# Performance work log

Measured on AMD Instinct MI355X. Metric: run time of the kernel, lower is better.

## Reference

```python
import jax, jax.numpy as jnp
import numpy as np

N_NODES = 100000   # type_num + rel_num
TYPE_NUM = 80000
EMB_DIM = 64
DIM1 = 64
DIM2 = 64
N_EDGES = 1_600_000


def _gcn_conv(x, W, b, src, dst, norm, n):
    # PyG GCNConv: h = x @ W, then symmetric-normalized aggregation, then bias
    h = x @ W                              # [n, out]
    msgs = norm[:, None] * h[src]          # [e, out] gather
    out = jax.ops.segment_sum(msgs, dst, num_segments=n)  # scatter-add
    return out + b


def setup_inputs() -> dict:
    key = jax.random.key(0)
    k0, k1, k2, k3 = jax.random.split(key, 4)
    # xavier-uniform style scales
    def xavier(k, shape):
        fan_in, fan_out = shape[-2], shape[-1]
        lim = float(np.sqrt(6.0 / (fan_in + fan_out)))
        return jax.random.uniform(k, shape, jnp.float32, -lim, lim)
    node_emb = xavier(k0, (N_NODES, EMB_DIM))
    W1 = xavier(k1, (EMB_DIM, DIM1))
    b1 = jnp.zeros((DIM1,), jnp.float32)
    W2 = xavier(k2, (DIM1, DIM2))
    b2 = jnp.zeros((DIM2,), jnp.float32)
    edge_index = jax.random.randint(k3, (2, N_EDGES), 0, N_NODES, dtype=jnp.int32)
    return {"node_emb": node_emb, "W1": W1, "b1": b1, "W2": W2, "b2": b2,
            "edge_index": edge_index}


def reference(node_emb, W1, b1, W2, b2, edge_index):
    n = node_emb.shape[0]
    # GCNConv default: add self-loops, symmetric normalization D^-1/2 (A+I) D^-1/2
    loops = jnp.arange(n, dtype=edge_index.dtype)
    src = jnp.concatenate([edge_index[0], loops])
    dst = jnp.concatenate([edge_index[1], loops])
    deg = jax.ops.segment_sum(jnp.ones_like(dst, dtype=node_emb.dtype), dst,
                              num_segments=n)
    dinv = jnp.where(deg > 0, jax.lax.rsqrt(deg), 0.0)
    norm = dinv[src] * dinv[dst]           # [e+n]
    X = jax.nn.relu(_gcn_conv(node_emb, W1, b1, src, dst, norm, n))
    X = jax.nn.relu(_gcn_conv(X, W2, b2, src, dst, norm, n))
    return X[:TYPE_NUM], X[TYPE_NUM:]
```

## Files before the change

kernel.cpp:

```cpp
#include <hip/hip_runtime.h>
#include <hip/hip_bf16.h>


#define BSH   7
#define BMSK  127
#define CAPE  2592
#define EPB   8192

__global__ __launch_bounds__(256) void k_part(const int* __restrict__ src,
                                              const int* __restrict__ dst,
                                              int* __restrict__ bcur,
                                              unsigned* __restrict__ tpack,
                                              int ne, int nb) {
    __shared__ int lh[800], lbase[800], lrk[800];
    for (int t = threadIdx.x; t < nb; t += 256) { lh[t] = 0; lrk[t] = 0; }
    __syncthreads();
    const int beg = blockIdx.x * EPB;
    const int end = min(beg + EPB, ne);
    for (int e = beg + threadIdx.x * 4; e < end; e += 1024) {
        if (e + 3 < end) {
            int4 d = *(const int4*)(dst + e);
            atomicAdd(&lh[d.x >> BSH], 1);
            atomicAdd(&lh[d.y >> BSH], 1);
            atomicAdd(&lh[d.z >> BSH], 1);
            atomicAdd(&lh[d.w >> BSH], 1);
        } else {
            for (int q = e; q < end; ++q) atomicAdd(&lh[dst[q] >> BSH], 1);
        }
    }
    __syncthreads();
    for (int t = threadIdx.x; t < nb; t += 256)
        lbase[t] = lh[t] ? atomicAdd(&bcur[t], lh[t]) : 0;
    __syncthreads();
    for (int e = beg + threadIdx.x * 4; e < end; e += 1024) {
        if (e + 3 < end) {
            int4 d4 = *(const int4*)(dst + e);
            int4 s4 = *(const int4*)(src + e);
            int b, r, pos;
            b = d4.x >> BSH; r = atomicAdd(&lrk[b], 1); pos = lbase[b] + r;
            if (pos < CAPE) tpack[(size_t)b * CAPE + pos] = (unsigned)s4.x | ((unsigned)(d4.x & BMSK) << 17);
            b = d4.y >> BSH; r = atomicAdd(&lrk[b], 1); pos = lbase[b] + r;
            if (pos < CAPE) tpack[(size_t)b * CAPE + pos] = (unsigned)s4.y | ((unsigned)(d4.y & BMSK) << 17);
            b = d4.z >> BSH; r = atomicAdd(&lrk[b], 1); pos = lbase[b] + r;
            if (pos < CAPE) tpack[(size_t)b * CAPE + pos] = (unsigned)s4.z | ((unsigned)(d4.z & BMSK) << 17);
            b = d4.w >> BSH; r = atomicAdd(&lrk[b], 1); pos = lbase[b] + r;
            if (pos < CAPE) tpack[(size_t)b * CAPE + pos] = (unsigned)s4.w | ((unsigned)(d4.w & BMSK) << 17);
        } else {
            for (int q = e; q < end; ++q) {
                int d = dst[q], s = src[q];
                int b = d >> BSH;
                int r = atomicAdd(&lrk[b], 1);
                int pos = lbase[b] + r;
                if (pos < CAPE) tpack[(size_t)b * CAPE + pos] = (unsigned)s | ((unsigned)(d & BMSK) << 17);
            }
        }
    }
}

__global__ __launch_bounds__(256) void k_bin(const unsigned* __restrict__ tpack,
                                             const int* __restrict__ bcur,
                                             int* __restrict__ offsets,
                                             int* __restrict__ ecnt,
                                             float* __restrict__ dinv,
                                             unsigned* __restrict__ ssort,
                                             const float* __restrict__ emb,
                                             float* __restrict__ Xe, int n) {
    __shared__ int hist[128], loff[128], cur[128];
    __shared__ float ldv[128];
    const int b = blockIdx.x;
    const int cnt = min(bcur[b], CAPE);
    const int dbase = b << BSH;
    const unsigned* tp = tpack + (size_t)b * CAPE;
    if (threadIdx.x < 128) { hist[threadIdx.x] = 0; cur[threadIdx.x] = 0; }
    __syncthreads();
    for (int e = threadIdx.x; e < cnt; e += 256)
        atomicAdd(&hist[tp[e] >> 17], 1);
    __syncthreads();
    if (threadIdx.x < 64) {
        const int lane = threadIdx.x;
        int v0 = hist[lane], v1 = hist[64 + lane];
        int x0 = v0, x1 = v1;
        #pragma unroll
        for (int off = 1; off < 64; off <<= 1) {
            int t0 = __shfl_up(x0, off); if (lane >= off) x0 += t0;
            int t1 = __shfl_up(x1, off); if (lane >= off) x1 += t1;
        }
        int sum0 = __shfl(x0, 63);
        loff[lane]      = x0 - v0;
        loff[64 + lane] = sum0 + x1 - v1;
    }
    __syncthreads();
    if (threadIdx.x < 128) {
        const int d = dbase + threadIdx.x;
        const float dv = rsqrtf((float)(hist[threadIdx.x] + 1));
        ldv[threadIdx.x] = dv;
        if (d < n) {
            offsets[d] = b * CAPE + loff[threadIdx.x];
            ecnt[d]    = hist[threadIdx.x];
            dinv[d]    = dv;
        }
    }
    __syncthreads();
    {
        const float4* ev = (const float4*)(emb + (size_t)dbase * 64);
        float4*       xv = (float4*)(Xe + (size_t)dbase * 64);
        const int lim = min(n - dbase, 128) * 16;
        for (int idx = threadIdx.x; idx < lim; idx += 256) {
            const float dv = ldv[idx >> 4];
            float4 v = ev[idx];
            v.x *= dv; v.y *= dv; v.z *= dv; v.w *= dv;
            xv[idx] = v;
        }
    }
    unsigned* sb = ssort + (size_t)b * CAPE;
    for (int e = threadIdx.x; e < cnt; e += 256) {
        unsigned p = tp[e];
        int dl = (int)(p >> 17);
        int r  = atomicAdd(&cur[dl], 1);
        sb[loff[dl] + r] = p & 0x1FFFFu;
    }
}

__global__ __launch_bounds__(256) void k_agg(const float* __restrict__ X,
                                             const int* __restrict__ offsets,
                                             const int* __restrict__ ecnt,
                                             const unsigned* __restrict__ ssort,
                                             const float* __restrict__ dinv,
                                             float* __restrict__ Y, int n) {
    __shared__ unsigned sw[16][48];
    const int g  = threadIdx.x >> 4;
    const int fl = threadIdx.x & 15;
    const int f0 = fl * 4;
    const int i  = blockIdx.x * 16 + g;
    if (i >= n) return;
    const int beg = offsets[i];
    const int cnt = ecnt[i];
    const float di = dinv[i];
    float4 acc = {0.f, 0.f, 0.f, 0.f};
    for (int cb = 0; cb < cnt; cb += 32) {
        const int ccnt = min(cnt - cb, 32);
        {
            const int t0 = fl, t1 = fl + 16;
            sw[g][t0] = (t0 < ccnt) ? ssort[beg + cb + t0] : 0u;
            sw[g][t1] = (t1 < ccnt) ? ssort[beg + cb + t1] : 0u;
        }
        for (int jb = 0; jb < ccnt; jb += 8) {
            unsigned p[8];
            #pragma unroll
            for (int u = 0; u < 8; ++u) p[u] = sw[g][jb + u];
            float4 h[8];
            #pragma unroll
            for (int u = 0; u < 8; ++u)
                h[u] = *(const float4*)(X + (size_t)p[u] * 64 + f0);
            #pragma unroll
            for (int u = 0; u < 8; ++u) {
                const float w = (jb + u < ccnt) ? 1.f : 0.f;
                acc.x = fmaf(w, h[u].x, acc.x);
                acc.y = fmaf(w, h[u].y, acc.y);
                acc.z = fmaf(w, h[u].z, acc.z);
                acc.w = fmaf(w, h[u].w, acc.w);
            }
        }
    }
    const float4 xs = *(const float4*)(X + (size_t)i * 64 + f0);
    acc.x = di * (acc.x + xs.x);
    acc.y = di * (acc.y + xs.y);
    acc.z = di * (acc.z + xs.z);
    acc.w = di * (acc.w + xs.w);
    *(float4*)(Y + (size_t)i * 64 + f0) = acc;
}

#define GEMM_ACC(ai, xi)                                                  \
    ai.x = fmaf(xi.x, w0.x, ai.x); ai.y = fmaf(xi.x, w0.y, ai.y);         \
    ai.z = fmaf(xi.x, w0.z, ai.z); ai.w = fmaf(xi.x, w0.w, ai.w);         \
    ai.x = fmaf(xi.y, w1.x, ai.x); ai.y = fmaf(xi.y, w1.y, ai.y);         \
    ai.z = fmaf(xi.y, w1.z, ai.z); ai.w = fmaf(xi.y, w1.w, ai.w);         \
    ai.x = fmaf(xi.z, w2.x, ai.x); ai.y = fmaf(xi.z, w2.y, ai.y);         \
    ai.z = fmaf(xi.z, w2.z, ai.z); ai.w = fmaf(xi.z, w2.w, ai.w);         \
    ai.x = fmaf(xi.w, w3.x, ai.x); ai.y = fmaf(xi.w, w3.y, ai.y);         \
    ai.z = fmaf(xi.w, w3.z, ai.z); ai.w = fmaf(xi.w, w3.w, ai.w);

#define GEMM_STORE(ai, idx)                                               \
    if (r0 + idx < n) {                                                   \
        float4 r;                                                         \
        r.x = fmaxf(ai.x + bv.x, 0.f); r.y = fmaxf(ai.y + bv.y, 0.f);     \
        r.z = fmaxf(ai.z + bv.z, 0.f); r.w = fmaxf(ai.w + bv.w, 0.f);     \
        if (SCALE) {                                                      \
            const float sc = rscale[r0 + idx];                            \
            r.x *= sc; r.y *= sc; r.z *= sc; r.w *= sc;                   \
        }                                                                 \
        *(float4*)(H + (size_t)(r0 + idx) * 64 + c0) = r;                 \
    }

template<bool SCALE>
__global__ __launch_bounds__(256, 4) void k_gemm64(const float* __restrict__ X,
                                                   const float* __restrict__ W,
                                                   const float* __restrict__ bias,
                                                   const float* __restrict__ rscale,
                                                   float* __restrict__ H, int n) {
    __shared__ float Wl[64 * 64];
    {
        const float4* Wv = (const float4*)W;
        float4* Wlv = (float4*)Wl;
        for (int t = threadIdx.x; t < 1024; t += 256) Wlv[t] = Wv[t];
    }
    __syncthreads();
    const int cg = threadIdx.x & 15;
    const int rg = threadIdx.x >> 4;
    const int c0 = cg * 4;
    const float4 bv = *(const float4*)(bias + c0);
    const int ntile = (n + 63) >> 6;
    for (int t = blockIdx.x; t < ntile; t += gridDim.x) {
        const int r0 = t * 64 + rg * 4;
        const float* xp0 = X + (size_t)min(r0 + 0, n - 1) * 64;
        const float* xp1 = X + (size_t)min(r0 + 1, n - 1) * 64;
        const float* xp2 = X + (size_t)min(r0 + 2, n - 1) * 64;
        const float* xp3 = X + (size_t)min(r0 + 3, n - 1) * 64;
        float4 a0 = {0,0,0,0}, a1 = {0,0,0,0}, a2 = {0,0,0,0}, a3 = {0,0,0,0};
        #pragma unroll 4
        for (int k = 0; k < 64; k += 4) {
            const float4 x0 = *(const float4*)(xp0 + k);
            const float4 x1 = *(const float4*)(xp1 + k);
            const float4 x2 = *(const float4*)(xp2 + k);
            const float4 x3 = *(const float4*)(xp3 + k);
            const float4 w0 = *(const float4*)(&Wl[(k + 0) * 64 + c0]);
            const float4 w1 = *(const float4*)(&Wl[(k + 1) * 64 + c0]);
            const float4 w2 = *(const float4*)(&Wl[(k + 2) * 64 + c0]);
            const float4 w3 = *(const float4*)(&Wl[(k + 3) * 64 + c0]);
            GEMM_ACC(a0, x0)
            GEMM_ACC(a1, x1)
            GEMM_ACC(a2, x2)
            GEMM_ACC(a3, x3)
        }
        GEMM_STORE(a0, 0)
        GEMM_STORE(a1, 1)
        GEMM_STORE(a2, 2)
        GEMM_STORE(a3, 3)
    }
}

extern "C" void kernel_launch(void* const* d_in, const int* in_sizes, int n_in,
                              void* d_out, int out_size, void* d_ws, size_t ws_size,
                              hipStream_t stream) {
    const float* emb = (const float*)d_in[0];
    const float* W1  = (const float*)d_in[1];
    const float* b1  = (const float*)d_in[2];
    const float* W2  = (const float*)d_in[3];
    const float* b2  = (const float*)d_in[4];
    const int*   ei  = (const int*)d_in[5];

    const int n  = in_sizes[0] / 64;
    const int ne = in_sizes[5] / 2;
    const int* src = ei;
    const int* dst = ei + ne;
    const int nb = (n + BMSK) >> BSH;

    char* ws = (char*)d_ws;
    size_t off = 0;
    auto alloc = [&](size_t bytes) { void* p = ws + off; off = (off + bytes + 63) & ~size_t(63); return p; };
    int*      bcur    = (int*)     alloc((size_t)nb * 4);
    int*      offsets = (int*)     alloc((size_t)n * 4);
    int*      ecnt    = (int*)     alloc((size_t)n * 4);
    float*    dinv    = (float*)   alloc((size_t)n * 4);
    unsigned* ssort   = (unsigned*)alloc((size_t)nb * CAPE * 4);
    size_t ybytes = (size_t)n * 64 * 4;
    size_t tbytes = (size_t)nb * CAPE * 4;
    void* yt = alloc(ybytes > tbytes ? ybytes : tbytes);
    unsigned* tpack = (unsigned*)yt;
    float*    Y     = (float*)yt;
    (void)ws_size;

    float* out = (float*)d_out;

    hipMemsetAsync(bcur, 0, (size_t)nb * 4, stream);

    const int pb = (ne + EPB - 1) / EPB;
    const int wb = (n + 15) / 16;
    const int gb = min((n + 63) / 64, 2048);

    k_part<<<pb, 256, 0, stream>>>(src, dst, bcur, tpack, ne, nb);
    k_bin <<<nb, 256, 0, stream>>>(tpack, bcur, offsets, ecnt, dinv, ssort,
                                   emb, out, n);

    k_agg<<<wb, 256, 0, stream>>>(out, offsets, ecnt, ssort, dinv, Y, n);
    k_gemm64<true><<<gb, 256, 0, stream>>>(Y, W1, b1, dinv, out, n);
    k_agg<<<wb, 256, 0, stream>>>(out, offsets, ecnt, ssort, dinv, Y, n);
    k_gemm64<false><<<gb, 256, 0, stream>>>(Y, W2, b2, nullptr, out, n);
}
```

Baseline: 208.3 us.

## Fuse neighbor aggregation with dense 64x64 transform in one kernel per layer

Merges the gather-aggregation kernel and the GEMM kernel into a single 1024-thread kernel per layer. The aggregated rows stay in shared memory and are multiplied by the weight tile loaded there, so the intermediate Y buffer is never written to or read back from global memory, and two launches are removed. In exchange, blocks are larger and carry more shared memory (weights, row tile and index staging), which can lower occupancy. The wave-skewed edge loop now sits before a block-wide barrier, so uneven degrees within a block leave threads idle.

```diff
diff --git a/kernel.cpp b/kernel.cpp
--- a/kernel.cpp
+++ b/kernel.cpp
@@ -121,121 +121,93 @@
     }
 }
 
-__global__ __launch_bounds__(256) void k_agg(const float* __restrict__ X,
-                                             const int* __restrict__ offsets,
-                                             const int* __restrict__ ecnt,
-                                             const unsigned* __restrict__ ssort,
-                                             const float* __restrict__ dinv,
-                                             float* __restrict__ Y, int n) {
-    __shared__ unsigned sw[16][48];
+template<bool SCALE>
+__global__ __launch_bounds__(1024, 8)
+void k_fused(const float* __restrict__ X,
+             const float* __restrict__ W,
+             const float* __restrict__ bias,
+             const float* __restrict__ rscale,
+             const int* __restrict__ offsets,
+             const int* __restrict__ ecnt,
+             const unsigned* __restrict__ ssort,
+             const float* __restrict__ dinv,
+             float* __restrict__ H, int n) {
+    __shared__ float    Wl[64 * 64];
+    __shared__ float    Xs[64][68];
+    __shared__ unsigned sw[64][48];
+    {
+        const float4* Wv = (const float4*)W;
+        float4* Wlv = (float4*)Wl;
+        Wlv[threadIdx.x] = Wv[threadIdx.x];
+    }
     const int g  = threadIdx.x >> 4;
     const int fl = threadIdx.x & 15;
     const int f0 = fl * 4;
-    const int i  = blockIdx.x * 16 + g;
-    if (i >= n) return;
-    const int beg = offsets[i];
-    const int cnt = ecnt[i];
-    const float di = dinv[i];
+    const int i  = blockIdx.x * 64 + g;
+
     float4 acc = {0.f, 0.f, 0.f, 0.f};
-    for (int cb = 0; cb < cnt; cb += 32) {
-        const int ccnt = min(cnt - cb, 32);
-        {
-            const int t0 = fl, t1 = fl + 16;
-            sw[g][t0] = (t0 < ccnt) ? ssort[beg + cb + t0] : 0u;
-            sw[g][t1] = (t1 < ccnt) ? ssort[beg + cb + t1] : 0u;
-        }
-        for (int jb = 0; jb < ccnt; jb += 8) {
-            unsigned p[8];
-            #pragma unroll
-            for (int u = 0; u < 8; ++u) p[u] = sw[g][jb + u];
-            float4 h[8];
-            #pragma unroll
-            for (int u = 0; u < 8; ++u)
-                h[u] = *(const float4*)(X + (size_t)p[u] * 64 + f0);
-            #pragma unroll
-            for (int u = 0; u < 8; ++u) {
-                const float w = (jb + u < ccnt) ? 1.f : 0.f;
-                acc.x = fmaf(w, h[u].x, acc.x);
-                acc.y = fmaf(w, h[u].y, acc.y);
-                acc.z = fmaf(w, h[u].z, acc.z);
-                acc.w = fmaf(w, h[u].w, acc.w);
+    if (i < n) {
+        const int beg = offsets[i];
+        const int cnt = ecnt[i];
+        const float di = dinv[i];
+        for (int cb = 0; cb < cnt; cb += 32) {
+            const int ccnt = min(cnt - cb, 32);
+            sw[g][fl]      = (fl      < ccnt) ? ssort[beg + cb + fl]      : 0u;
+            sw[g][fl + 16] = (fl + 16 < ccnt) ? ssort[beg + cb + fl + 16] : 0u;
+            for (int jb = 0; jb < ccnt; jb += 8) {
+                unsigned p[8];
+                #pragma unroll
+                for (int u = 0; u < 8; ++u) p[u] = sw[g][jb + u];
+                float4 h[8];
+                #pragma unroll
+                for (int u = 0; u < 8; ++u)
+                    h[u] = *(const float4*)(X + (size_t)p[u] * 64 + f0);
+                #pragma unroll
+                for (int u = 0; u < 8; ++u) {
+                    const float w = (jb + u < ccnt) ? 1.f : 0.f;
+                    acc.x = fmaf(w, h[u].x, acc.x);
+                    acc.y = fmaf(w, h[u].y, acc.y);
+                    acc.z = fmaf(w, h[u].z, acc.z);
+                    acc.w = fmaf(w, h[u].w, acc.w);
+                }
             }
         }
-    }
-    const float4 xs = *(const float4*)(X + (size_t)i * 64 + f0);
-    acc.x = di * (acc.x + xs.x);
-    acc.y = di * (acc.y + xs.y);
-    acc.z = di * (acc.z + xs.z);
-    acc.w = di * (acc.w + xs.w);
-    *(float4*)(Y + (size_t)i * 64 + f0) = acc;
-}
-
-#define GEMM_ACC(ai, xi)                                                  \
-    ai.x = fmaf(xi.x, w0.x, ai.x); ai.y = fmaf(xi.x, w0.y, ai.y);         \
-    ai.z = fmaf(xi.x, w0.z, ai.z); ai.w = fmaf(xi.x, w0.w, ai.w);         \
-    ai.x = fmaf(xi.y, w1.x, ai.x); ai.y = fmaf(xi.y, w1.y, ai.y);         \
-    ai.z = fmaf(xi.y, w1.z, ai.z); ai.w = fmaf(xi.y, w1.w, ai.w);         \
-    ai.x = fmaf(xi.z, w2.x, ai.x); ai.y = fmaf(xi.z, w2.y, ai.y);         \
-    ai.z = fmaf(xi.z, w2.z, ai.z); ai.w = fmaf(xi.z, w2.w, ai.w);         \
-    ai.x = fmaf(xi.w, w3.x, ai.x); ai.y = fmaf(xi.w, w3.y, ai.y);         \
-    ai.z = fmaf(xi.w, w3.z, ai.z); ai.w = fmaf(xi.w, w3.w, ai.w);
-
-#define GEMM_STORE(ai, idx)                                               \
-    if (r0 + idx < n) {                                                   \
-        float4 r;                                                         \
-        r.x = fmaxf(ai.x + bv.x, 0.f); r.y = fmaxf(ai.y + bv.y, 0.f);     \
-        r.z = fmaxf(ai.z + bv.z, 0.f); r.w = fmaxf(ai.w + bv.w, 0.f);     \
-        if (SCALE) {                                                      \
-            const float sc = rscale[r0 + idx];                            \
-            r.x *= sc; r.y *= sc; r.z *= sc; r.w *= sc;                   \
-        }                                                                 \
-        *(float4*)(H + (size_t)(r0 + idx) * 64 + c0) = r;                 \
-    }
-
-template<bool SCALE>
-__global__ __launch_bounds__(256, 4) void k_gemm64(const float* __restrict__ X,
-                                                   const float* __restrict__ W,
-                                                   const float* __restrict__ bias,
-                                                   const float* __restrict__ rscale,
-                                                   float* __restrict__ H, int n) {
-    __shared__ float Wl[64 * 64];
-    {
-        const float4* Wv = (const float4*)W;
-        float4* Wlv = (float4*)Wl;
-        for (int t = threadIdx.x; t < 1024; t += 256) Wlv[t] = Wv[t];
-    }
-    __syncthreads();
-    const int cg = threadIdx.x & 15;
-    const int rg = threadIdx.x >> 4;
-    const int c0 = cg * 4;
-    const float4 bv = *(const float4*)(bias + c0);
-    const int ntile = (n + 63) >> 6;
-    for (int t = blockIdx.x; t < ntile; t += gridDim.x) {
-        const int r0 = t * 64 + rg * 4;
-        const float* xp0 = X + (size_t)min(r0 + 0, n - 1) * 64;
-        const float* xp1 = X + (size_t)min(r0 + 1, n - 1) * 64;
-        const float* xp2 = X + (size_t)min(r0 + 2, n - 1) * 64;
-        const float* xp3 = X + (size_t)min(r0 + 3, n - 1) * 64;
-        float4 a0 = {0,0,0,0}, a1 = {0,0,0,0}, a2 = {0,0,0,0}, a3 = {0,0,0,0};
-        #pragma unroll 4
-        for (int k = 0; k < 64; k += 4) {
-            const float4 x0 = *(const float4*)(xp0 + k);
-            const float4 x1 = *(const float4*)(xp1 + k);
-            const float4 x2 = *(const float4*)(xp2 + k);
-            const float4 x3 = *(const float4*)(xp3 + k);
-            const float4 w0 = *(const float4*)(&Wl[(k + 0) * 64 + c0]);
-            const float4 w1 = *(const float4*)(&Wl[(k + 1) * 64 + c0]);
-            const float4 w2 = *(const float4*)(&Wl[(k + 2) * 64 + c0]);
-            const float4 w3 = *(const float4*)(&Wl[(k + 3) * 64 + c0]);
-            GEMM_ACC(a0, x0)
-            GEMM_ACC(a1, x1)
-            GEMM_ACC(a2, x2)
-            GEMM_ACC(a3, x3)
-        }
-        GEMM_STORE(a0, 0)
-        GEMM_STORE(a1, 1)
-        GEMM_STORE(a2, 2)
-        GEMM_STORE(a3, 3)
+        const float4 xs = *(const float4*)(X + (size_t)i * 64 + f0);
+        acc.x = di * (acc.x + xs.x);
+        acc.y = di * (acc.y + xs.y);
+        acc.z = di * (acc.z + xs.z);
+        acc.w = di * (acc.w + xs.w);
+    }
+    *(float4*)(&Xs[g][f0]) = acc;
+    __syncthreads();
+
+    const float4 bv = *(const float4*)(bias + f0);
+    float4 a = {0.f, 0.f, 0.f, 0.f};
+    #pragma unroll 4
+    for (int k = 0; k < 64; k += 4) {
+        const float4 x4 = *(const float4*)(&Xs[g][k]);
+        const float4 w0 = *(const float4*)(&Wl[(k + 0) * 64 + f0]);
+        const float4 w1 = *(const float4*)(&Wl[(k + 1) * 64 + f0]);
+        const float4 w2 = *(const float4*)(&Wl[(k + 2) * 64 + f0]);
+        const float4 w3 = *(const float4*)(&Wl[(k + 3) * 64 + f0]);
+        a.x = fmaf(x4.x, w0.x, a.x); a.y = fmaf(x4.x, w0.y, a.y);
+        a.z = fmaf(x4.x, w0.z, a.z); a.w = fmaf(x4.x, w0.w, a.w);
+        a.x = fmaf(x4.y, w1.x, a.x); a.y = fmaf(x4.y, w1.y, a.y);
+        a.z = fmaf(x4.y, w1.z, a.z); a.w = fmaf(x4.y, w1.w, a.w);
+        a.x = fmaf(x4.z, w2.x, a.x); a.y = fmaf(x4.z, w2.y, a.y);
+        a.z = fmaf(x4.z, w2.z, a.z); a.w = fmaf(x4.z, w2.w, a.w);
+        a.x = fmaf(x4.w, w3.x, a.x); a.y = fmaf(x4.w, w3.y, a.y);
+        a.z = fmaf(x4.w, w3.z, a.z); a.w = fmaf(x4.w, w3.w, a.w);
+    }
+    if (i < n) {
+        float4 r;
+        r.x = fmaxf(a.x + bv.x, 0.f); r.y = fmaxf(a.y + bv.y, 0.f);
+        r.z = fmaxf(a.z + bv.z, 0.f); r.w = fmaxf(a.w + bv.w, 0.f);
+        if (SCALE) {
+            const float sc = rscale[i];
+            r.x *= sc; r.y *= sc; r.z *= sc; r.w *= sc;
+        }
+        *(float4*)(H + (size_t)i * 64 + f0) = r;
     }
 }
 
@@ -267,7 +239,7 @@
     size_t tbytes = (size_t)nb * CAPE * 4;
     void* yt = alloc(ybytes > tbytes ? ybytes : tbytes);
     unsigned* tpack = (unsigned*)yt;
-    float*    Y     = (float*)yt;
+    float*    X2    = (float*)yt;
     (void)ws_size;
 
     float* out = (float*)d_out;
@@ -275,15 +247,14 @@
     hipMemsetAsync(bcur, 0, (size_t)nb * 4, stream);
 
     const int pb = (ne + EPB - 1) / EPB;
-    const int wb = (n + 15) / 16;
-    const int gb = min((n + 63) / 64, 2048);
+    const int fb = (n + 63) / 64;
 
     k_part<<<pb, 256, 0, stream>>>(src, dst, bcur, tpack, ne, nb);
     k_bin <<<nb, 256, 0, stream>>>(tpack, bcur, offsets, ecnt, dinv, ssort,
                                    emb, out, n);
 
-    k_agg<<<wb, 256, 0, stream>>>(out, offsets, ecnt, ssort, dinv, Y, n);
-    k_gemm64<true><<<gb, 256, 0, stream>>>(Y, W1, b1, dinv, out, n);
-    k_agg<<<wb, 256, 0, stream>>>(out, offsets, ecnt, ssort, dinv, Y, n);
-    k_gemm64<false><<<gb, 256, 0, stream>>>(Y, W2, b2, nullptr, out, n);
-}
+    k_fused<true><<<fb, 1024, 0, stream>>>(out, W1, b1, dinv,
+                                           offsets, ecnt, ssort, dinv, X2, n);
+    k_fused<false><<<fb, 1024, 0, stream>>>(X2, W2, b2, nullptr,
+                                            offsets, ecnt, ssort, dinv, out, n);
+}
```

New measurement: 212.1 us. About the same (+1.8%).
